# Kernel tuning notes

Hardware: AMD Instinct MI355X
Metric: run time of the kernel (lower is better)

## Reference

```python
import jax, jax.numpy as jnp
import numpy as np

SAMPLES = 160000  # 10 s at 16 kHz
BATCH = 32
RIR_LEN = 16000   # 1 s RIR


def _make_rir(key, length=RIR_LEN):
    # Mirrors _generate_synthetic_rir: exponentially decaying noise, direct path = 1.
    t = jnp.linspace(0.0, 1.0, length)
    decay = jnp.exp(-5.0 * t)
    rir = jax.random.normal(key, (length,), dtype=jnp.float32) * decay
    rir = rir.at[0].set(1.0)
    # a few discrete reflections (fixed positions for determinism)
    for pos, amp in [(1200, 0.4), (4500, 0.3), (9000, 0.2), (13000, 0.15)]:
        rir = rir.at[pos].add(amp * (1.0 - pos / length))
    return rir / jnp.max(jnp.abs(rir))


def setup_inputs() -> dict:
    key = jax.random.key(0)
    k1, k2 = jax.random.split(key)
    waveform = jax.random.normal(k1, (BATCH, SAMPLES), dtype=jnp.float32)
    rir = _make_rir(k2)
    return {"waveform": waveform, "rir": rir}


def reference(waveform, rir):
    # waveform: [B, S], rir: [K]
    K = rir.shape[0]
    x = waveform[:, None, :]          # [B, 1, S]  (NCW)
    kern = rir[None, None, :]         # [O=1, I=1, K]
    # F.conv1d is cross-correlation; lax.conv_general_dilated matches (no kernel flip).
    # Left-pad K-1 zeros -> output length S (causal FIR).
    y = jax.lax.conv_general_dilated(
        x, kern, window_strides=(1,), padding=[(K - 1, 0)],
        dimension_numbers=("NCH", "OIH", "NCH"))
    y = y[:, 0, :]                    # [B, S]
    return y / (jnp.max(jnp.abs(y)) + 1e-8)
```

## Files before the change

kernel.cpp:

```cpp
#include <hip/hip_runtime.h>
#include <stdint.h>


#define T_LEN   160000
#define BATCH   32
#define K_LEN   16000
#define NCHUNK  1002
#define NCHUNK_PAD 1004
#define BPR     20
#define BLK_OUT 8192
#define NST     (K_LEN + BLK_OUT)
#define NST8    (NST / 8)
#define LY_PITCH 33

typedef __attribute__((ext_vector_type(8)))  short short8;
typedef __attribute__((ext_vector_type(16))) float f32x16;

__device__ __forceinline__ unsigned swz(unsigned b) {
  return b ^ (((b >> 7) & 7u) << 4);
}

__device__ __forceinline__ short f2bf(float f) {
  unsigned u = __float_as_uint(f);
  u += 0x7fffu + ((u >> 16) & 1u);
  return (short)(u >> 16);
}

__global__ __launch_bounds__(256) void build_atab_k(
    const float* __restrict__ rir, short8* __restrict__ atab, unsigned* __restrict__ wsmax)
{
  int tid = blockIdx.x * 256 + threadIdx.x;
  if (tid == 0) *wsmax = 0u;
  if (tid >= NCHUNK_PAD * 64) return;
  int j = tid >> 6, l = tid & 63;
  int m = l & 31, h = l >> 5;
  int d = 16 * j - 16;
  short8 o;
  #pragma unroll
  for (int e = 0; e < 8; ++e) {
    int k = d + m - (8 * h + e);
    float v = (k >= 0 && k < K_LEN) ? rir[K_LEN - 1 - k] : 0.0f;
    o[e] = f2bf(v);
  }
  atab[tid] = o;
}

__device__ __forceinline__ short8 lds_rd(const char* smem, int elem) {
  int byte = elem * 2;
  byte = byte < 0 ? 0 : byte;
  return *(const short8*)(smem + swz((unsigned)byte));
}

__global__ __launch_bounds__(256, 3) void conv_k(
    const float* __restrict__ x, const short8* __restrict__ atab,
    float* __restrict__ out, unsigned* __restrict__ wsmax)
{
  __shared__ __align__(16) char smem[NST * 2];
  __shared__ float wmaxs[4];

  int blk  = blockIdx.x;
  int brow = blk / BPR;
  int tb   = (blk - brow * BPR) * BLK_OUT;
  const float* __restrict__ xrow = x + (size_t)brow * T_LEN;
  int s_base = tb - K_LEN;
  int tid = threadIdx.x;

  for (int i = tid; i < NST8; i += 256) {
    int s = s_base + i * 8;
    float v[8];
    if (s >= 0 && s + 8 <= T_LEN) {
      float4 a0 = *(const float4*)(xrow + s);
      float4 a1 = *(const float4*)(xrow + s + 4);
      v[0]=a0.x; v[1]=a0.y; v[2]=a0.z; v[3]=a0.w;
      v[4]=a1.x; v[5]=a1.y; v[6]=a1.z; v[7]=a1.w;
    } else {
      #pragma unroll
      for (int e = 0; e < 8; ++e) {
        int se = s + e;
        v[e] = (se >= 0 && se < T_LEN) ? xrow[se] : 0.0f;
      }
    }
    short8 hv;
    #pragma unroll
    for (int e = 0; e < 8; ++e) hv[e] = f2bf(v[e]);
    *(short8*)(smem + swz((unsigned)(i * 16))) = hv;
  }
  __syncthreads();

  int l  = tid & 63;
  int w  = tid >> 6;
  int q  = l & 31;
  int hh = l >> 5;

  f32x16 acc00, acc01, acc10, acc11;
  #pragma unroll
  for (int r = 0; r < 16; ++r) { acc00[r]=0.f; acc01[r]=0.f; acc10[r]=0.f; acc11[r]=0.f; }

  const short8* ap = atab + l;
  int base0 = (K_LEN + 16) + 2048 * w + 32 * q + 8 * hh;

  short8 a0 = ap[0];
  short8 a1 = ap[64];
  short8 b00 = lds_rd(smem, base0);
  short8 b01 = lds_rd(smem, base0 + 1024);
  short8 b10 = lds_rd(smem, base0 - 16);
  short8 b11 = lds_rd(smem, base0 + 1024 - 16);

  for (int s = 0; s < NCHUNK; s += 2) {
    short8 a0n = ap[(s + 2) * 64];
    short8 a1n = ap[(s + 3) * 64];
    int e2 = base0 - 16 * (s + 2);
    short8 b00n = lds_rd(smem, e2);
    short8 b01n = lds_rd(smem, e2 + 1024);
    short8 b10n = lds_rd(smem, e2 - 16);
    short8 b11n = lds_rd(smem, e2 + 1024 - 16);

    acc00 = __builtin_amdgcn_mfma_f32_32x32x16_bf16(a0, b00, acc00, 0, 0, 0);
    acc01 = __builtin_amdgcn_mfma_f32_32x32x16_bf16(a0, b01, acc01, 0, 0, 0);
    acc10 = __builtin_amdgcn_mfma_f32_32x32x16_bf16(a1, b10, acc10, 0, 0, 0);
    acc11 = __builtin_amdgcn_mfma_f32_32x32x16_bf16(a1, b11, acc11, 0, 0, 0);

    a0 = a0n; a1 = a1n; b00 = b00n; b01 = b01n; b10 = b10n; b11 = b11n;
  }
  __syncthreads();

  float* ly = (float*)smem + w * (32 * LY_PITCH);
  float lm = 0.0f;
  const float* __restrict__ orow_c = out + (size_t)brow * T_LEN;
  float* __restrict__ orow = (float*)orow_c;

  #pragma unroll
  for (int b = 0; b < 2; ++b) {
    f32x16 v;
    #pragma unroll
    for (int r = 0; r < 16; ++r)
      v[r] = (b == 0 ? acc00[r] + acc10[r] : acc01[r] + acc11[r]);
    #pragma unroll
    for (int r = 0; r < 16; ++r) {
      int m = (r & 3) + 8 * (r >> 2) + 4 * hh;
      ly[q * LY_PITCH + m] = v[r];
    }
    int tbase = tb + 2048 * w + 1024 * b;
    #pragma unroll
    for (int p = 0; p < 4; ++p) {
      int t_loc = 256 * p + 4 * l;
      int t = tbase + t_loc;
      if (t < T_LEN) {
        int phys = (t_loc >> 5) * LY_PITCH + (t_loc & 31);
        float4 o4;
        o4.x = ly[phys + 0]; o4.y = ly[phys + 1]; o4.z = ly[phys + 2]; o4.w = ly[phys + 3];
        *(float4*)(orow + t) = o4;
        lm = fmaxf(lm, fmaxf(fmaxf(fabsf(o4.x), fabsf(o4.y)), fmaxf(fabsf(o4.z), fabsf(o4.w))));
      }
    }
  }

  #pragma unroll
  for (int off = 32; off; off >>= 1) lm = fmaxf(lm, __shfl_xor(lm, off));
  if (l == 0) wmaxs[w] = lm;
  __syncthreads();
  if (tid == 0) {
    float m4 = fmaxf(fmaxf(wmaxs[0], wmaxs[1]), fmaxf(wmaxs[2], wmaxs[3]));
    atomicMax(wsmax, __float_as_uint(m4));
  }
}

__global__ __launch_bounds__(256) void normalize_k(
    float* __restrict__ out, const unsigned* __restrict__ wsmax, int n4)
{
  float mx = __uint_as_float(*wsmax);
  float s = 1.0f / (mx + 1e-8f);
  int stride = gridDim.x * blockDim.x;
  for (int i = blockIdx.x * blockDim.x + threadIdx.x; i < n4; i += stride) {
    float4 v = ((const float4*)out)[i];
    v.x *= s; v.y *= s; v.z *= s; v.w *= s;
    ((float4*)out)[i] = v;
  }
}

extern "C" void kernel_launch(void* const* d_in, const int* in_sizes, int n_in,
                              void* d_out, int out_size, void* d_ws, size_t ws_size,
                              hipStream_t stream) {
  const float* wav = (const float*)d_in[0];
  const float* rir = (const float*)d_in[1];
  float* outp      = (float*)d_out;
  unsigned* wsmax  = (unsigned*)d_ws;
  short8* atab     = (short8*)((char*)d_ws + 256);

  hipLaunchKernelGGL(build_atab_k, dim3((NCHUNK_PAD * 64 + 255) / 256), dim3(256), 0, stream,
                     rir, atab, wsmax);
  hipLaunchKernelGGL(conv_k, dim3(BATCH * BPR), dim3(256), 0, stream,
                     wav, atab, outp, wsmax);
  hipLaunchKernelGGL(normalize_k, dim3(1280), dim3(256), 0, stream,
                     outp, wsmax, (BATCH * T_LEN) / 4);
}
```

Before: 243.6 us.

## Use 2x2 MFMA register tiling with 2-wave blocks for operand reuse

Restructures the MFMA inner loop so each wave computes 4096 outputs with a 2x2 tile: two Toeplitz A fragments (offset by 64 chunks) are each reused against two LDS B fragments. Before, each A fragment was used twice and each B fragment once. The loop now runs 1066 steps per wave instead of 501 double-steps. Blocks shrink to 128 threads and the A table grows with front padding so out-of-range chunks read zeros. This lowers LDS and global loads per MFMA, at the cost of fewer waves per block, less latency hiding, and some extra zero-padded MFMA work.

```diff
diff --git a/kernel.cpp b/kernel.cpp
--- a/kernel.cpp
+++ b/kernel.cpp
@@ -5,12 +5,13 @@
 #define T_LEN   160000
 #define BATCH   32
 #define K_LEN   16000
-#define NCHUNK  1002
-#define NCHUNK_PAD 1004
+#define NCHUNK_TAB 1132
 #define BPR     20
 #define BLK_OUT 8192
-#define NST     (K_LEN + BLK_OUT)
+#define FPAD    32
+#define NST     (K_LEN + BLK_OUT + FPAD)
 #define NST8    (NST / 8)
+#define NSTEP   1066
 #define LY_PITCH 33
 
 typedef __attribute__((ext_vector_type(8)))  short short8;
@@ -26,15 +27,19 @@
   return (short)(u >> 16);
 }
 
+__device__ __forceinline__ short8 lds_rd(const char* smem, int elem) {
+  return *(const short8*)(smem + swz((unsigned)(elem * 2)));
+}
+
 __global__ __launch_bounds__(256) void build_atab_k(
     const float* __restrict__ rir, short8* __restrict__ atab, unsigned* __restrict__ wsmax)
 {
   int tid = blockIdx.x * 256 + threadIdx.x;
   if (tid == 0) *wsmax = 0u;
-  if (tid >= NCHUNK_PAD * 64) return;
-  int j = tid >> 6, l = tid & 63;
+  if (tid >= NCHUNK_TAB * 64) return;
+  int jj = tid >> 6, l = tid & 63;
   int m = l & 31, h = l >> 5;
-  int d = 16 * j - 16;
+  int d = 16 * (jj - 64) - 16;
   short8 o;
   #pragma unroll
   for (int e = 0; e < 8; ++e) {
@@ -45,27 +50,21 @@
   atab[tid] = o;
 }
 
-__device__ __forceinline__ short8 lds_rd(const char* smem, int elem) {
-  int byte = elem * 2;
-  byte = byte < 0 ? 0 : byte;
-  return *(const short8*)(smem + swz((unsigned)byte));
-}
-
-__global__ __launch_bounds__(256, 3) void conv_k(
+__global__ __launch_bounds__(128) void conv_k(
     const float* __restrict__ x, const short8* __restrict__ atab,
     float* __restrict__ out, unsigned* __restrict__ wsmax)
 {
   __shared__ __align__(16) char smem[NST * 2];
-  __shared__ float wmaxs[4];
+  __shared__ float wmaxs[2];
 
   int blk  = blockIdx.x;
   int brow = blk / BPR;
   int tb   = (blk - brow * BPR) * BLK_OUT;
   const float* __restrict__ xrow = x + (size_t)brow * T_LEN;
-  int s_base = tb - K_LEN;
+  int s_base = tb - K_LEN - FPAD;
   int tid = threadIdx.x;
 
-  for (int i = tid; i < NST8; i += 256) {
+  for (int i = tid; i < NST8; i += 128) {
     int s = s_base + i * 8;
     float v[8];
     if (s >= 0 && s + 8 <= T_LEN) {
@@ -92,55 +91,48 @@
   int q  = l & 31;
   int hh = l >> 5;
 
-  f32x16 acc00, acc01, acc10, acc11;
+  f32x16 acc0, acc1, acc2, acc3;
   #pragma unroll
-  for (int r = 0; r < 16; ++r) { acc00[r]=0.f; acc01[r]=0.f; acc10[r]=0.f; acc11[r]=0.f; }
+  for (int r = 0; r < 16; ++r) { acc0[r]=0.f; acc1[r]=0.f; acc2[r]=0.f; acc3[r]=0.f; }
 
   const short8* ap = atab + l;
-  int base0 = (K_LEN + 16) + 2048 * w + 32 * q + 8 * hh;
+  int C2 = FPAD + K_LEN + 16 + 1024 + 4096 * w + 32 * q + 8 * hh;
 
-  short8 a0 = ap[0];
-  short8 a1 = ap[64];
-  short8 b00 = lds_rd(smem, base0);
-  short8 b01 = lds_rd(smem, base0 + 1024);
-  short8 b10 = lds_rd(smem, base0 - 16);
-  short8 b11 = lds_rd(smem, base0 + 1024 - 16);
+  short8 aa  = ap[0];
+  short8 ab  = ap[64 * 64];
+  short8 blo = lds_rd(smem, C2);
+  short8 bhi = lds_rd(smem, C2 + 2048);
 
-  for (int s = 0; s < NCHUNK; s += 2) {
-    short8 a0n = ap[(s + 2) * 64];
-    short8 a1n = ap[(s + 3) * 64];
-    int e2 = base0 - 16 * (s + 2);
-    short8 b00n = lds_rd(smem, e2);
-    short8 b01n = lds_rd(smem, e2 + 1024);
-    short8 b10n = lds_rd(smem, e2 - 16);
-    short8 b11n = lds_rd(smem, e2 + 1024 - 16);
+  #pragma unroll 2
+  for (int ss = 0; ss < NSTEP; ++ss) {
+    short8 aan = ap[(ss + 1) * 64];
+    short8 abn = ap[(ss + 65) * 64];
+    int e = C2 - 16 * (ss + 1);
+    short8 blon = lds_rd(smem, e);
+    short8 bhin = lds_rd(smem, e + 2048);
 
-    acc00 = __builtin_amdgcn_mfma_f32_32x32x16_bf16(a0, b00, acc00, 0, 0, 0);
-    acc01 = __builtin_amdgcn_mfma_f32_32x32x16_bf16(a0, b01, acc01, 0, 0, 0);
-    acc10 = __builtin_amdgcn_mfma_f32_32x32x16_bf16(a1, b10, acc10, 0, 0, 0);
-    acc11 = __builtin_amdgcn_mfma_f32_32x32x16_bf16(a1, b11, acc11, 0, 0, 0);
+    acc0 = __builtin_amdgcn_mfma_f32_32x32x16_bf16(aa, blo, acc0, 0, 0, 0);
+    acc1 = __builtin_amdgcn_mfma_f32_32x32x16_bf16(ab, blo, acc1, 0, 0, 0);
+    acc2 = __builtin_amdgcn_mfma_f32_32x32x16_bf16(aa, bhi, acc2, 0, 0, 0);
+    acc3 = __builtin_amdgcn_mfma_f32_32x32x16_bf16(ab, bhi, acc3, 0, 0, 0);
 
-    a0 = a0n; a1 = a1n; b00 = b00n; b01 = b01n; b10 = b10n; b11 = b11n;
+    aa = aan; ab = abn; blo = blon; bhi = bhin;
   }
   __syncthreads();
 
   float* ly = (float*)smem + w * (32 * LY_PITCH);
   float lm = 0.0f;
-  const float* __restrict__ orow_c = out + (size_t)brow * T_LEN;
-  float* __restrict__ orow = (float*)orow_c;
+  float* __restrict__ orow = out + (size_t)brow * T_LEN;
 
   #pragma unroll
-  for (int b = 0; b < 2; ++b) {
-    f32x16 v;
-    #pragma unroll
-    for (int r = 0; r < 16; ++r)
-      v[r] = (b == 0 ? acc00[r] + acc10[r] : acc01[r] + acc11[r]);
+  for (int b = 0; b < 4; ++b) {
+    f32x16 v = (b == 0) ? acc0 : (b == 1) ? acc1 : (b == 2) ? acc2 : acc3;
     #pragma unroll
     for (int r = 0; r < 16; ++r) {
       int m = (r & 3) + 8 * (r >> 2) + 4 * hh;
       ly[q * LY_PITCH + m] = v[r];
     }
-    int tbase = tb + 2048 * w + 1024 * b;
+    int tbase = tb + 4096 * w + 1024 * b;
     #pragma unroll
     for (int p = 0; p < 4; ++p) {
       int t_loc = 256 * p + 4 * l;
@@ -159,10 +151,7 @@
   for (int off = 32; off; off >>= 1) lm = fmaxf(lm, __shfl_xor(lm, off));
   if (l == 0) wmaxs[w] = lm;
   __syncthreads();
-  if (tid == 0) {
-    float m4 = fmaxf(fmaxf(wmaxs[0], wmaxs[1]), fmaxf(wmaxs[2], wmaxs[3]));
-    atomicMax(wsmax, __float_as_uint(m4));
-  }
+  if (tid == 0) atomicMax(wsmax, __float_as_uint(fmaxf(wmaxs[0], wmaxs[1])));
 }
 
 __global__ __launch_bounds__(256) void normalize_k(
@@ -187,9 +176,9 @@
   unsigned* wsmax  = (unsigned*)d_ws;
   short8* atab     = (short8*)((char*)d_ws + 256);
 
-  hipLaunchKernelGGL(build_atab_k, dim3((NCHUNK_PAD * 64 + 255) / 256), dim3(256), 0, stream,
+  hipLaunchKernelGGL(build_atab_k, dim3((NCHUNK_TAB * 64 + 255) / 256), dim3(256), 0, stream,
                      rir, atab, wsmax);
-  hipLaunchKernelGGL(conv_k, dim3(BATCH * BPR), dim3(256), 0, stream,
+  hipLaunchKernelGGL(conv_k, dim3(BATCH * BPR), dim3(128), 0, stream,
                      wav, atab, outp, wsmax);
   hipLaunchKernelGGL(normalize_k, dim3(1280), dim3(256), 0, stream,
                      outp, wsmax, (BATCH * T_LEN) / 4);
```

After: 294.0 us. 20.7% more time.
